# Performance work log

Hardware: AMD Instinct MI355X
Metric: run time of the kernel (lower is better)

## Reference

```python
import jax, jax.numpy as jnp
import numpy as np

B, L, T = 32, 256, 32
V_SIZE, D, H = 30000, 300, 256


def _gru(x, h0, Wih, Whh, bih, bhh):
    # x: [B,S,D], h0: [B,H]; PyTorch GRU gate order: r, z, n
    xg = jnp.einsum('bsd,gd->bsg', x, Wih) + bih  # [B,S,3H]

    def step(h, xg_t):
        gh = jnp.einsum('bh,gh->bg', h, Whh) + bhh
        ir, iz, in_ = jnp.split(xg_t, 3, axis=-1)
        hr, hz, hn_ = jnp.split(gh, 3, axis=-1)
        r = jax.nn.sigmoid(ir + hr)
        z = jax.nn.sigmoid(iz + hz)
        n = jnp.tanh(in_ + r * hn_)
        h_new = (1.0 - z) * n + z * h
        return h_new, h_new

    h_last, outs = jax.lax.scan(step, h0, jnp.swapaxes(xg, 0, 1))
    return jnp.swapaxes(outs, 0, 1), h_last  # [B,S,H], [B,H]


def setup_inputs() -> dict:
    rng = np.random.default_rng(0)
    Xin = rng.integers(0, V_SIZE, (B, L)).astype(np.int64)
    # strictly increasing segment ends; starts = previous end + 1
    Yindex = np.stack([np.sort(rng.choice(L, T, replace=False)) for _ in range(B)]).astype(np.int64)
    Xindex = np.concatenate([np.zeros((B, 1), np.int64), Yindex[:, :-1] + 1], axis=1)
    lens = np.full((B,), L, np.int64)
    s = 0.05
    p = lambda *shape: jnp.asarray(rng.standard_normal(shape) * s, jnp.float32)
    return {
        'Xin': jnp.asarray(Xin), 'Xindex': jnp.asarray(Xindex),
        'Yindex': jnp.asarray(Yindex), 'lens': jnp.asarray(lens),
        'emb': jnp.asarray(rng.standard_normal((V_SIZE, D)) * 0.1, jnp.float32),
        'Wih_e': p(3 * H, D), 'Whh_e': p(3 * H, H), 'bih_e': p(3 * H), 'bhh_e': p(3 * H),
        'Wih_d': p(3 * H, D), 'Whh_d': p(3 * H, H), 'bih_d': p(3 * H), 'bhh_d': p(3 * H),
        'W1': p(H, H), 'W2': p(H, H), 'Vv': p(H),
    }


def reference(Xin, Xindex, Yindex, lens, emb, Wih_e, Whh_e, bih_e, bhh_e,
              Wih_d, Whh_d, bih_d, bhh_d, W1, W2, Vv):
    # pointerEncoder (isbanor=False, dropout=0, lens==L so packed == plain)
    X = emb[Xin]                                   # [B,L,D]
    h0 = jnp.zeros((Xin.shape[0], Whh_e.shape[1]), X.dtype)
    hn, h_end = _gru(X, h0, Wih_e, Whh_e, bih_e, bhh_e)  # [B,L,H],[B,H]
    # training_decoder, vectorized over batch and decode steps
    dec_tok = jnp.take_along_axis(Xin, Xindex, axis=1)   # token ids at segment starts
    dx = emb[dec_tok]                              # [B,T,D]
    dout, _ = _gru(dx, h_end, Wih_d, Whh_d, bih_d, bhh_d)  # [B,T,H]
    # pointerLayer: v = selu(V . selu(W1 en + W2 d)), masked log_softmax over [start, curL)
    WE = jnp.einsum('blh,kh->blk', hn, W1)         # [B,L,H]
    WD = jnp.einsum('bth,kh->btk', dout, W2)       # [B,T,H]
    s = jax.nn.selu(WE[:, None, :, :] + WD[:, :, None, :])  # [B,T,L,H]
    v = jax.nn.selu(jnp.einsum('btlh,h->btl', s, Vv))        # [B,T,L]
    pos = jnp.arange(hn.shape[1])
    mask = (pos[None, None, :] >= Xindex[:, :, None]) & (pos[None, None, :] < lens[:, None, None])
    logits = jnp.where(mask, v, -jnp.inf)
    logp = jax.nn.log_softmax(logits, axis=-1)
    tgt_logp = jnp.take_along_axis(logp, Yindex[:, :, None], axis=-1)[..., 0]  # [B,T]
    return -jnp.mean(tgt_logp)  # batch_loss / LoopN
```

## Files before the change

kernel.cpp:

```cpp
#include <hip/hip_runtime.h>
#include <hip/hip_bf16.h>
#include <stdint.h>

#define B_  32
#define L_  256
#define T_  32
#define D_  300
#define H_  256
#define G3  768

__device__ __forceinline__ int sdot4(uint32_t a, uint32_t b, int acc) {
#if defined(__has_builtin) && __has_builtin(__builtin_amdgcn_sdot4)
  return __builtin_amdgcn_sdot4((int)a, (int)b, acc, false);
#else
  const int a0 = (int)(signed char)(a & 0xff),  b0 = (int)(signed char)(b & 0xff);
  const int a1 = (int)(signed char)((a >> 8) & 0xff),  b1 = (int)(signed char)((b >> 8) & 0xff);
  const int a2 = (int)(signed char)((a >> 16) & 0xff), b2 = (int)(signed char)((b >> 16) & 0xff);
  const int a3 = (int)(signed char)(a >> 24),          b3 = (int)(signed char)(b >> 24);
  return acc + a0 * b0 + a1 * b1 + a2 * b2 + a3 * b3;
#endif
}

__device__ __forceinline__ int sdot8(uint32_t a, uint32_t b, int acc) {
#if defined(__has_builtin) && __has_builtin(__builtin_amdgcn_sdot8)
  return __builtin_amdgcn_sdot8((int)a, (int)b, acc, false);
#else
  const uint32_t M = 0xF0F0F0F0u;
  const uint32_t alo = (a << 4) & M, ahi = a & M;
  const uint32_t blo = (b << 4) & M, bhi = b & M;
  return acc + ((sdot4(alo, blo, 0) + sdot4(ahi, bhi, 0)) >> 8);
#endif
}

__device__ __forceinline__ float rcp_f(float x) { return __builtin_amdgcn_rcpf(x); }
__device__ __forceinline__ float sigmoid_f(float x) { return rcp_f(1.0f + __expf(-x)); }
__device__ __forceinline__ float tanh_f(float x) {
  float e2 = __expf(2.0f * x);
  return 1.0f - 2.0f * rcp_f(e2 + 1.0f);
}
__device__ __forceinline__ uint16_t f2bf(float x) {
  uint32_t u = __builtin_bit_cast(uint32_t, x);
  return (uint16_t)((u + 0x7FFF + ((u >> 16) & 1)) >> 16);
}
__device__ __forceinline__ float bf2f(uint16_t b) {
  uint32_t u = ((uint32_t)b) << 16;
  return __builtin_bit_cast(float, u);
}

__device__ __forceinline__ void pack_body(int blk, const float* __restrict__ Whh,
                                          uint32_t* __restrict__ wQ,
                                          float* __restrict__ sw) {
  const int row = blk * 4 + (threadIdx.x >> 6);
  const int lane = threadIdx.x & 63;
  const float* wr = Whh + (long)row * H_;
  float m = 0.0f;
#pragma unroll
  for (int u = 0; u < 4; ++u) m = fmaxf(m, fabsf(wr[lane + 64 * u]));
  for (int off = 32; off > 0; off >>= 1) m = fmaxf(m, __shfl_xor(m, off, 64));
  const float inv = m > 0.0f ? 7.0f / m : 0.0f;
  if (lane == 0) sw[row] = m > 0.0f ? m / 49.0f : 0.0f;
  if (lane < 32) {
    const int pd = lane;
    uint32_t d = 0;
#pragma unroll
    for (int jn = 0; jn < 8; ++jn) {
      int v = __float2int_rn(wr[8 * pd + jn] * inv);
      v = v > 7 ? 7 : (v < -7 ? -7 : v);
      d |= ((uint32_t)(v & 0xF)) << (4 * jn);
    }
    wQ[(((size_t)(pd >> 2) * G3 + row) << 2) + (pd & 3)] = d;
  }
}

__device__ __forceinline__ void quant_body(int blk, const float* __restrict__ A,
                                           const int* __restrict__ rowidx,
                                           const int* __restrict__ Xin2,
                                           const int* __restrict__ Xidx2,
                                           uint32_t* __restrict__ out,
                                           float* __restrict__ scale,
                                           int M, int K, int Kd) {
  const int row = blk * 4 + (threadIdx.x >> 6);
  const int lane = threadIdx.x & 63;
  if (row >= M) return;
  long src = row;
  if (rowidx) src = rowidx[row];
  else if (Xin2) src = Xin2[(row >> 5) * L_ + Xidx2[row]];
  const float* ar = A + src * (long)K;
  float m = 0.0f;
  for (int e = lane; e < K; e += 64) m = fmaxf(m, fabsf(ar[e]));
  for (int off = 32; off > 0; off >>= 1) m = fmaxf(m, __shfl_xor(m, off, 64));
  const float inv = m > 0.0f ? 127.0f / m : 0.0f;
  if (lane == 0) scale[row] = m * (1.0f / 127.0f);
  for (int kd = lane; kd < Kd; kd += 64) {
    uint32_t d = 0;
#pragma unroll
    for (int u = 0; u < 4; ++u) {
      const int e = 4 * kd + u;
      int qv = (e < K) ? __float2int_rn(ar[e] * inv) : 0;
      qv = qv > 127 ? 127 : (qv < -127 ? -127 : qv);
      d |= ((uint32_t)(qv & 0xff)) << (8 * u);
    }
    out[(long)row * Kd + kd] = d;
  }
}

__device__ __forceinline__ void quant16(int blk, const float* __restrict__ A,
                                        uint32_t* __restrict__ out,
                                        float* __restrict__ scale,
                                        int M, int K, int Kd) {
  const int row = blk * 16 + (threadIdx.x >> 6);
  const int lane = threadIdx.x & 63;
  if (row >= M) return;
  const float* ar = A + (long)row * K;
  float m = 0.0f;
  for (int e = lane; e < K; e += 64) m = fmaxf(m, fabsf(ar[e]));
  for (int off = 32; off > 0; off >>= 1) m = fmaxf(m, __shfl_xor(m, off, 64));
  const float inv = m > 0.0f ? 127.0f / m : 0.0f;
  if (lane == 0) scale[row] = m * (1.0f / 127.0f);
  for (int kd = lane; kd < Kd; kd += 64) {
    uint32_t d = 0;
#pragma unroll
    for (int u = 0; u < 4; ++u) {
      const int e = 4 * kd + u;
      int qv = (e < K) ? __float2int_rn(ar[e] * inv) : 0;
      qv = qv > 127 ? 127 : (qv < -127 ? -127 : qv);
      d |= ((uint32_t)(qv & 0xff)) << (8 * u);
    }
    out[(long)row * Kd + kd] = d;
  }
}

__global__ __launch_bounds__(256)
void prep_all(const float* __restrict__ Whh_e, const float* __restrict__ Whh_d,
              uint32_t* __restrict__ wQ_e, uint32_t* __restrict__ wQ_d,
              float* __restrict__ sw_e, float* __restrict__ sw_d,
              const float* __restrict__ Wih_e, const float* __restrict__ Wih_d,
              uint32_t* __restrict__ WihQ_e, uint32_t* __restrict__ WihQ_d,
              float* __restrict__ sWih_e, float* __restrict__ sWih_d,
              const float* __restrict__ W1, const float* __restrict__ W2,
              uint32_t* __restrict__ W1q, uint32_t* __restrict__ W2q,
              float* __restrict__ sW1, float* __restrict__ sW2,
              const float* __restrict__ emb, const int* __restrict__ Xin,
              const int* __restrict__ Xindex,
              uint32_t* __restrict__ Aqe, float* __restrict__ saAe,
              uint32_t* __restrict__ Aqd, float* __restrict__ saAd,
              const float* __restrict__ bih_e, const float* __restrict__ bhh_e,
              float* __restrict__ bsum_e,
              const float* __restrict__ bih_d, const float* __restrict__ bhh_d,
              float* __restrict__ bsum_d) {
  const int blk = blockIdx.x;
  if (blk < 192)        pack_body(blk, Whh_e, wQ_e, sw_e);
  else if (blk < 384)   pack_body(blk - 192, Whh_d, wQ_d, sw_d);
  else if (blk < 576)   quant_body(blk - 384, Wih_e, nullptr, nullptr, nullptr,
                                   WihQ_e, sWih_e, 768, 300, 80);
  else if (blk < 768)   quant_body(blk - 576, Wih_d, nullptr, nullptr, nullptr,
                                   WihQ_d, sWih_d, 768, 300, 80);
  else if (blk < 832)   quant_body(blk - 768, W1, nullptr, nullptr, nullptr,
                                   W1q, sW1, 256, 256, 64);
  else if (blk < 896)   quant_body(blk - 832, W2, nullptr, nullptr, nullptr,
                                   W2q, sW2, 256, 256, 64);
  else if (blk < 2944)  quant_body(blk - 896, emb, Xin, nullptr, nullptr,
                                   Aqe, saAe, 8192, 300, 80);
  else if (blk < 3200)  quant_body(blk - 2944, emb, nullptr, Xin, Xindex,
                                   Aqd, saAd, 1024, 300, 80);
  else {
    const int blk2 = blk - 3200;
    const int i = (blk2 % 3) * 256 + threadIdx.x;
    const float* bih = blk2 < 3 ? bih_e : bih_d;
    const float* bhh = blk2 < 3 ? bhh_e : bhh_d;
    float* bsum = blk2 < 3 ? bsum_e : bsum_d;
    float v = bih[i];
    if (i < 2 * H_) v += bhh[i];
    bsum[i] = v;
  }
}

__device__ __forceinline__
void gemm_body(const uint32_t* __restrict__ Aq, const float* __restrict__ sa,
               const uint32_t* __restrict__ Wq, const float* __restrict__ swc,
               const float* __restrict__ bias, void* __restrict__ C,
               int bm, int bn, int M, int N, int Kd,
               bool transp, bool biasF, bool bf16out) {
  __shared__ uint32_t As[8][68];
  __shared__ uint32_t Ws[8][68];
  const int tid = threadIdx.x;
  const int ty = tid >> 4, tx = tid & 15;
  const int srow = tid >> 2;
  const int skd = (tid & 3) << 1;
  const uint32_t* Arow = Aq + (long)(bm * 64 + srow) * Kd + skd;
  const uint32_t* Wrow = Wq + (long)(bn * 64 + srow) * Kd + skd;
  int acc[4][4] = {};
  for (int k0 = 0; k0 < Kd; k0 += 8) {
    const uint32_t a0 = Arow[k0], a1 = Arow[k0 + 1];
    const uint32_t w0 = Wrow[k0], w1 = Wrow[k0 + 1];
    __syncthreads();
    As[skd][srow] = a0; As[skd + 1][srow] = a1;
    Ws[skd][srow] = w0; Ws[skd + 1][srow] = w1;
    __syncthreads();
#pragma unroll
    for (int kd = 0; kd < 8; ++kd) {
      const uint4 a4 = *(const uint4*)&As[kd][ty << 2];
      const uint4 b4 = *(const uint4*)&Ws[kd][tx << 2];
      acc[0][0] = sdot4(a4.x, b4.x, acc[0][0]);
      acc[0][1] = sdot4(a4.x, b4.y, acc[0][1]);
      acc[0][2] = sdot4(a4.x, b4.z, acc[0][2]);
      acc[0][3] = sdot4(a4.x, b4.w, acc[0][3]);
      acc[1][0] = sdot4(a4.y, b4.x, acc[1][0]);
      acc[1][1] = sdot4(a4.y, b4.y, acc[1][1]);
      acc[1][2] = sdot4(a4.y, b4.z, acc[1][2]);
      acc[1][3] = sdot4(a4.y, b4.w, acc[1][3]);
      acc[2][0] = sdot4(a4.z, b4.x, acc[2][0]);
      acc[2][1] = sdot4(a4.z, b4.y, acc[2][1]);
      acc[2][2] = sdot4(a4.z, b4.z, acc[2][2]);
      acc[2][3] = sdot4(a4.z, b4.w, acc[2][3]);
      acc[3][0] = sdot4(a4.w, b4.x, acc[3][0]);
      acc[3][1] = sdot4(a4.w, b4.y, acc[3][1]);
      acc[3][2] = sdot4(a4.w, b4.z, acc[3][2]);
      acc[3][3] = sdot4(a4.w, b4.w, acc[3][3]);
    }
  }
#pragma unroll
  for (int i = 0; i < 4; ++i) {
    const int m = bm * 64 + (ty << 2) + i;
    const float sai = sa[m];
#pragma unroll
    for (int j = 0; j < 4; ++j) {
      const int n = bn * 64 + (tx << 2) + j;
      float v = (float)acc[i][j] * sai * swc[n];
      if (biasF) v += bias[n];
      const long idx = transp ? ((((long)(m >> 8) * N + n) << 8) + (m & 255))
                              : ((long)m * N + n);
      if (bf16out) ((uint16_t*)C)[idx] = f2bf(v);
      else         ((float*)C)[idx] = v;
    }
  }
}

__global__ __launch_bounds__(256)
void xg_gemms(const uint32_t* __restrict__ Aqe, const float* __restrict__ saAe,
              const uint32_t* __restrict__ WihQ_e, const float* __restrict__ sWih_e,
              const float* __restrict__ bsum_e, uint16_t* __restrict__ xg_e,
              const uint32_t* __restrict__ Aqd, const float* __restrict__ saAd,
              const uint32_t* __restrict__ WihQ_d, const float* __restrict__ sWih_d,
              const float* __restrict__ bsum_d, uint16_t* __restrict__ xg_d) {
  const int blk = blockIdx.x;
  if (blk < 1536)
    gemm_body(Aqe, saAe, WihQ_e, sWih_e, bsum_e, xg_e,
              blk % 128, blk / 128, 8192, 768, 80, false, true, true);
  else {
    const int k = blk - 1536;
    gemm_body(Aqd, saAd, WihQ_d, sWih_d, bsum_d, xg_d,
              k % 16, k / 16, 1024, 768, 80, false, true, true);
  }
}


#define DOT8V(acc, p_, h_) { \
  acc = sdot8(p_.x, h_.x, acc); acc = sdot8(p_.y, h_.y, acc); \
  acc = sdot8(p_.z, h_.z, acc); acc = sdot8(p_.w, h_.w, acc); }

__device__ __forceinline__
void gru_block(int b, const uint16_t* __restrict__ xg, const uint4* __restrict__ wQv,
               const float* __restrict__ sw, const float* __restrict__ bhh,
               const float* __restrict__ h0, float* __restrict__ hout,
               float* __restrict__ hlast, int S,
               uint32_t (*h2)[32], int4 (*partv)[H_]) {
  const int tid = threadIdx.x;
  const int j = tid & 255;
  const int q = tid >> 8;
  const int base = (q * 2) * G3 + j;
  float bhn = 0.0f, h = 0.0f, swr = 0.0f, swz = 0.0f, swn = 0.0f;
  const uint16_t* xp = xg + (long)b * S * G3;
  float* hp_out = hout + (long)b * S * H_;
  if (q == 0) {
    bhn = bhh[2 * H_ + j];
    swr = sw[j]; swz = sw[H_ + j]; swn = sw[2 * H_ + j];
    h = h0 ? h0[b * H_ + j] : 0.0f;
    int hq4 = __float2int_rn(h * 7.0f);
    hq4 = hq4 > 7 ? 7 : (hq4 < -7 ? -7 : hq4);
    const int hq4n = __shfl_down(hq4, 1, 64);
    if (!(j & 1))
      ((uint8_t*)h2[0])[j >> 1] = (uint8_t)((hq4 & 0xF) | ((hq4n & 0xF) << 4));
  }
  __syncthreads();
  for (int t = 0; t < S; ++t) {
    const uint4* hq = (const uint4*)h2[t & 1] + q * 2;
    const uint4 ha = hq[0], hb = hq[1];
    float xr = 0.0f, xz = 0.0f, xn = 0.0f;
    if (q == 0) {
      xr = bf2f(xp[j]); xz = bf2f(xp[H_ + j]); xn = bf2f(xp[2 * H_ + j]);
    }
    int ar = 0, az = 0, an = 0;
    {
      const uint4 p0 = wQv[base], p1 = wQv[base + G3];
      DOT8V(ar, p0, ha) DOT8V(ar, p1, hb)
    }
    {
      const uint4 p0 = wQv[base + H_], p1 = wQv[base + G3 + H_];
      DOT8V(az, p0, ha) DOT8V(az, p1, hb)
    }
    {
      const uint4 p0 = wQv[base + 2 * H_], p1 = wQv[base + G3 + 2 * H_];
      DOT8V(an, p0, ha) DOT8V(an, p1, hb)
    }
    if (q) partv[q][j] = make_int4(ar, az, an, 0);
    __syncthreads();
    if (q == 0) {
      const int4 p1 = partv[1][j];
      const int4 p2 = partv[2][j];
      const int4 p3 = partv[3][j];
      const float arf = (float)(ar + p1.x + p2.x + p3.x) * swr;
      const float azf = (float)(az + p1.y + p2.y + p3.y) * swz;
      const float anf = (float)(an + p1.z + p2.z + p3.z) * swn;
      const float r = sigmoid_f(xr + arf);
      const float z = sigmoid_f(xz + azf);
      const float n = tanh_f(xn + r * (anf + bhn));
      h = (1.0f - z) * n + z * h;
      hp_out[j] = h;
      int hq4 = __float2int_rn(h * 7.0f);
      hq4 = hq4 > 7 ? 7 : (hq4 < -7 ? -7 : hq4);
      const int hq4n = __shfl_down(hq4, 1, 64);
      if (!(j & 1))
        ((uint8_t*)h2[(t & 1) ^ 1])[j >> 1] =
            (uint8_t)((hq4 & 0xF) | ((hq4n & 0xF) << 4));
    }
    xp += G3;
    hp_out += H_;
    __syncthreads();
  }
  if (q == 0 && hlast) hlast[b * H_ + j] = h;
}

__global__ __launch_bounds__(1024)
void gru_enc(const uint16_t* __restrict__ xg, const uint4* __restrict__ wQv,
             const float* __restrict__ sw, const float* __restrict__ bhh,
             float* __restrict__ hout, float* __restrict__ hlast, int S) {
  __shared__ __align__(16) uint32_t h2[2][32];
  __shared__ int4 partv[4][H_];
  gru_block(blockIdx.x, xg, wQv, sw, bhh, nullptr, hout, hlast, S, h2, partv);
}

__global__ __launch_bounds__(1024)
void dec_and_hquant(const uint16_t* __restrict__ xg_d, const uint4* __restrict__ wQ_d,
                    const float* __restrict__ sw_d, const float* __restrict__ bhh_d,
                    const float* __restrict__ hend, float* __restrict__ doutb,
                    const float* __restrict__ hn, uint32_t* __restrict__ hnq,
                    float* __restrict__ sahn) {
  __shared__ __align__(16) uint32_t h2[2][32];
  __shared__ int4 partv[4][H_];
  if (blockIdx.x < 32)
    gru_block(blockIdx.x, xg_d, wQ_d, sw_d, bhh_d, hend, doutb,
              (float*)nullptr, T_, h2, partv);
  else
    quant16(blockIdx.x - 32, hn, hnq, sahn, 8192, 256, 64);
}

__global__ __launch_bounds__(256)
void wet_and_dquant(const uint32_t* __restrict__ hnq, const float* __restrict__ sahn,
                    const uint32_t* __restrict__ W1q, const float* __restrict__ sW1,
                    float* __restrict__ WEt,
                    const float* __restrict__ doutb, uint32_t* __restrict__ dq,
                    float* __restrict__ sad) {
  if (blockIdx.x < 512)
    gemm_body(hnq, sahn, W1q, sW1, nullptr, WEt,
              blockIdx.x & 127, blockIdx.x >> 7, 8192, 256, 64, true, false, false);
  else
    quant_body(blockIdx.x - 512, doutb, nullptr, nullptr, nullptr,
               dq, sad, 1024, 256, 64);
}

__global__ __launch_bounds__(256)
void wd_gemm(const uint32_t* __restrict__ dq, const float* __restrict__ sad,
             const uint32_t* __restrict__ W2q, const float* __restrict__ sW2,
             float* __restrict__ WDb) {
  gemm_body(dq, sad, W2q, sW2, nullptr, WDb,
            blockIdx.x & 15, blockIdx.x >> 4, 1024, 256, 64, false, false, false);
}

__global__ __launch_bounds__(256)
void pointer_loss(const float* __restrict__ WEt, const float* __restrict__ WD,
                  const float* __restrict__ Vv,
                  const int* __restrict__ Xindex, const int* __restrict__ Yindex,
                  const int* __restrict__ lens, float* __restrict__ out) {
  const int t = blockIdx.x, b = blockIdx.y;
  const int l = threadIdx.x;
  __shared__ float wd_s[H_], vv_s[H_];
  __shared__ float rbuf[4], sbuf[4], vy_s;
  const int bt = b * T_ + t;
  wd_s[l] = WD[(long)bt * H_ + l];
  vv_s[l] = Vv[l] * 1.0507009873554805f;
  __syncthreads();
  const float* wet = WEt + (long)b * H_ * L_;
  const float alpha = 1.6732632423543772f;
  float acc = 0.0f;
#pragma unroll 4
  for (int hh = 0; hh < H_; ++hh) {
    const float xsum = wet[hh * L_ + l] + wd_s[hh];
    const float sneg = alpha * (__expf(xsum) - 1.0f);
    const float s = xsum > 0.0f ? xsum : sneg;
    acc = fmaf(s, vv_s[hh], acc);
  }
  float v;
  {
    const float sneg = alpha * (__expf(acc) - 1.0f);
    v = 1.0507009873554805f * (acc > 0.0f ? acc : sneg);
  }
  const int start = Xindex[bt];
  const int len = lens[b];
  const bool valid = (l >= start) && (l < len);
  const int y = Yindex[bt];
  if (l == y) vy_s = v;
  float m = valid ? v : -INFINITY;
  for (int off = 32; off > 0; off >>= 1) m = fmaxf(m, __shfl_xor(m, off, 64));
  const int wid = l >> 6, lane = l & 63;
  if (lane == 0) rbuf[wid] = m;
  __syncthreads();
  const float mx = fmaxf(fmaxf(rbuf[0], rbuf[1]), fmaxf(rbuf[2], rbuf[3]));
  float e = valid ? __expf(v - mx) : 0.0f;
  for (int off = 32; off > 0; off >>= 1) e += __shfl_xor(e, off, 64);
  if (lane == 0) sbuf[wid] = e;
  __syncthreads();
  if (l == 0) {
    const float sum = sbuf[0] + sbuf[1] + sbuf[2] + sbuf[3];
    atomicAdd(out, (mx + __logf(sum) - vy_s) * (1.0f / (B_ * T_)));
  }
}

extern "C" void kernel_launch(void* const* d_in, const int* in_sizes, int n_in,
                              void* d_out, int out_size, void* d_ws, size_t ws_size,
                              hipStream_t stream) {
  (void)in_sizes; (void)n_in; (void)out_size; (void)ws_size;
  const int*   Xin    = (const int*)d_in[0];
  const int*   Xindex = (const int*)d_in[1];
  const int*   Yindex = (const int*)d_in[2];
  const int*   lens   = (const int*)d_in[3];
  const float* emb    = (const float*)d_in[4];
  const float* Wih_e  = (const float*)d_in[5];
  const float* Whh_e  = (const float*)d_in[6];
  const float* bih_e  = (const float*)d_in[7];
  const float* bhh_e  = (const float*)d_in[8];
  const float* Wih_d  = (const float*)d_in[9];
  const float* Whh_d  = (const float*)d_in[10];
  const float* bih_d  = (const float*)d_in[11];
  const float* bhh_d  = (const float*)d_in[12];
  const float* W1     = (const float*)d_in[13];
  const float* W2     = (const float*)d_in[14];
  const float* Vv     = (const float*)d_in[15];

  char* p = (char*)d_ws;
  auto take = [&](size_t bytes) { void* q = (void*)p; p += (bytes + 255) & ~(size_t)255; return q; };
  uint32_t* wQ_e   = (uint32_t*)take((size_t)32 * G3 * 4);
  uint32_t* wQ_d   = (uint32_t*)take((size_t)32 * G3 * 4);
  float*    sw_e   = (float*)take((size_t)768 * 4);
  float*    sw_d   = (float*)take((size_t)768 * 4);
  uint32_t* WihQ_e = (uint32_t*)take((size_t)768 * 80 * 4);
  uint32_t* WihQ_d = (uint32_t*)take((size_t)768 * 80 * 4);
  float*    sWih_e = (float*)take((size_t)768 * 4);
  float*    sWih_d = (float*)take((size_t)768 * 4);
  uint32_t* W1q    = (uint32_t*)take((size_t)256 * 64 * 4);
  uint32_t* W2q    = (uint32_t*)take((size_t)256 * 64 * 4);
  float*    sW1    = (float*)take((size_t)256 * 4);
  float*    sW2    = (float*)take((size_t)256 * 4);
  float*    bsum_e = (float*)take((size_t)768 * 4);
  float*    bsum_d = (float*)take((size_t)768 * 4);
  uint16_t* xg_e   = (uint16_t*)take((size_t)8192 * 768 * 2);
  uint16_t* xg_d   = (uint16_t*)take((size_t)1024 * 768 * 2);
  float*    hn     = (float*)take((size_t)8192 * 256 * 4);
  float*    hend   = (float*)take((size_t)8192 * 4);
  float*    doutb  = (float*)take((size_t)1024 * 256 * 4);
  float*    WDb    = (float*)take((size_t)1024 * 256 * 4);
  float*    WEt    = (float*)take((size_t)8192 * 256 * 4);
  uint32_t* Aqe    = (uint32_t*)take((size_t)8192 * 80 * 4);
  float*    saAe   = (float*)take((size_t)8192 * 4);
  uint32_t* Aqd    = (uint32_t*)take((size_t)1024 * 80 * 4);
  float*    saAd   = (float*)take((size_t)1024 * 4);
  uint32_t* hnq  = Aqe;
  float*    sahn = saAe;
  uint32_t* dq   = Aqd;
  float*    sad  = saAd;

  hipMemsetAsync(d_out, 0, sizeof(float), stream);

  hipLaunchKernelGGL(prep_all, dim3(3206), dim3(256), 0, stream,
                     Whh_e, Whh_d, wQ_e, wQ_d, sw_e, sw_d,
                     Wih_e, Wih_d, WihQ_e, WihQ_d, sWih_e, sWih_d,
                     W1, W2, W1q, W2q, sW1, sW2,
                     emb, Xin, Xindex, Aqe, saAe, Aqd, saAd,
                     bih_e, bhh_e, bsum_e, bih_d, bhh_d, bsum_d);

  hipLaunchKernelGGL(xg_gemms, dim3(1728), dim3(256), 0, stream,
                     Aqe, saAe, WihQ_e, sWih_e, bsum_e, xg_e,
                     Aqd, saAd, WihQ_d, sWih_d, bsum_d, xg_d);

  hipLaunchKernelGGL(gru_enc, dim3(32), dim3(1024), 0, stream,
                     xg_e, (const uint4*)wQ_e, sw_e, bhh_e, hn, hend, L_);

  hipLaunchKernelGGL(dec_and_hquant, dim3(544), dim3(1024), 0, stream,
                     xg_d, (const uint4*)wQ_d, sw_d, bhh_d, hend, doutb,
                     hn, hnq, sahn);

  hipLaunchKernelGGL(wet_and_dquant, dim3(768), dim3(256), 0, stream,
                     hnq, sahn, W1q, sW1, WEt, doutb, dq, sad);

  hipLaunchKernelGGL(wd_gemm, dim3(64), dim3(256), 0, stream,
                     dq, sad, W2q, sW2, WDb);

  hipLaunchKernelGGL(pointer_loss, dim3(T_, B_), dim3(256), 0, stream,
                     WEt, WDb, Vv, Xindex, Yindex, lens, (float*)d_out);
}
```

Before: 285.8 us.

## Double-buffer GRU weight registers and use LDS-only barriers in recurrent loop

Unrolls the GRU time loop by two and ping-pongs two register sets of quantized Whh weights, issuing the next step's weight loads before the current step's dot products. This hides global or L2 load latency behind compute. Barriers now wait only on lgkmcnt before s_barrier, so outstanding global loads need not drain at each sync. A large unused shared array in the encoder kernel limits occupancy to one block per CU, likely to give each sequential GRU block its own CU. The weights are loop-invariant, so the repeated loads are redundant but kept, and the unroll assumes S is even.

```diff
diff --git a/kernel.cpp b/kernel.cpp
--- a/kernel.cpp
+++ b/kernel.cpp
@@ -259,6 +259,49 @@
   acc = sdot8(p_.x, h_.x, acc); acc = sdot8(p_.y, h_.y, acc); \
   acc = sdot8(p_.z, h_.z, acc); acc = sdot8(p_.w, h_.w, acc); }
 
+#define LGKM_BARRIER() { \
+  asm volatile("s_waitcnt lgkmcnt(0)" ::: "memory"); \
+  __builtin_amdgcn_s_barrier(); }
+
+#define GRU_STEP(CUR, NXT, TT) { \
+  NXT##r0 = wp[0];        NXT##r1 = wp[G3]; \
+  NXT##z0 = wp[H_];       NXT##z1 = wp[G3 + H_]; \
+  NXT##n0 = wp[2 * H_];   NXT##n1 = wp[G3 + 2 * H_]; \
+  const uint4* hq_ = (const uint4*)h2[(TT) & 1] + q * 2; \
+  const uint4 ha_ = hq_[0], hb_ = hq_[1]; \
+  float xr_ = 0.0f, xz_ = 0.0f, xn_ = 0.0f; \
+  if (q == 0) { \
+    xr_ = bf2f(xp[j]); xz_ = bf2f(xp[H_ + j]); xn_ = bf2f(xp[2 * H_ + j]); \
+  } \
+  int ar_ = 0, az_ = 0, an_ = 0; \
+  DOT8V(ar_, CUR##r0, ha_) DOT8V(ar_, CUR##r1, hb_) \
+  DOT8V(az_, CUR##z0, ha_) DOT8V(az_, CUR##z1, hb_) \
+  DOT8V(an_, CUR##n0, ha_) DOT8V(an_, CUR##n1, hb_) \
+  if (q) partv[q][j] = make_int4(ar_, az_, an_, 0); \
+  LGKM_BARRIER(); \
+  if (q == 0) { \
+    const int4 p1_ = partv[1][j]; \
+    const int4 p2_ = partv[2][j]; \
+    const int4 p3_ = partv[3][j]; \
+    const float arf_ = (float)(ar_ + p1_.x + p2_.x + p3_.x) * swr; \
+    const float azf_ = (float)(az_ + p1_.y + p2_.y + p3_.y) * swz; \
+    const float anf_ = (float)(an_ + p1_.z + p2_.z + p3_.z) * swn; \
+    const float r_ = sigmoid_f(xr_ + arf_); \
+    const float z_ = sigmoid_f(xz_ + azf_); \
+    const float n_ = tanh_f(xn_ + r_ * (anf_ + bhn)); \
+    h = (1.0f - z_) * n_ + z_ * h; \
+    hp_out[j] = h; \
+    int hq4_ = __float2int_rn(h * 7.0f); \
+    hq4_ = hq4_ > 7 ? 7 : (hq4_ < -7 ? -7 : hq4_); \
+    const int hq4n_ = __shfl_down(hq4_, 1, 64); \
+    if (!(j & 1)) \
+      ((uint8_t*)h2[((TT) & 1) ^ 1])[j >> 1] = \
+          (uint8_t)((hq4_ & 0xF) | ((hq4n_ & 0xF) << 4)); \
+  } \
+  xp += G3; \
+  hp_out += H_; \
+  LGKM_BARRIER(); }
+
 __device__ __forceinline__
 void gru_block(int b, const uint16_t* __restrict__ xg, const uint4* __restrict__ wQv,
                const float* __restrict__ sw, const float* __restrict__ bhh,
@@ -268,7 +311,7 @@
   const int tid = threadIdx.x;
   const int j = tid & 255;
   const int q = tid >> 8;
-  const int base = (q * 2) * G3 + j;
+  const uint4* wp = wQv + (q * 2) * G3 + j;
   float bhn = 0.0f, h = 0.0f, swr = 0.0f, swz = 0.0f, swn = 0.0f;
   const uint16_t* xp = xg + (long)b * S * G3;
   float* hp_out = hout + (long)b * S * H_;
@@ -282,51 +325,14 @@
     if (!(j & 1))
       ((uint8_t*)h2[0])[j >> 1] = (uint8_t)((hq4 & 0xF) | ((hq4n & 0xF) << 4));
   }
+  uint4 uAr0 = wp[0],      uAr1 = wp[G3];
+  uint4 uAz0 = wp[H_],     uAz1 = wp[G3 + H_];
+  uint4 uAn0 = wp[2 * H_], uAn1 = wp[G3 + 2 * H_];
+  uint4 uBr0, uBr1, uBz0, uBz1, uBn0, uBn1;
   __syncthreads();
-  for (int t = 0; t < S; ++t) {
-    const uint4* hq = (const uint4*)h2[t & 1] + q * 2;
-    const uint4 ha = hq[0], hb = hq[1];
-    float xr = 0.0f, xz = 0.0f, xn = 0.0f;
-    if (q == 0) {
-      xr = bf2f(xp[j]); xz = bf2f(xp[H_ + j]); xn = bf2f(xp[2 * H_ + j]);
-    }
-    int ar = 0, az = 0, an = 0;
-    {
-      const uint4 p0 = wQv[base], p1 = wQv[base + G3];
-      DOT8V(ar, p0, ha) DOT8V(ar, p1, hb)
-    }
-    {
-      const uint4 p0 = wQv[base + H_], p1 = wQv[base + G3 + H_];
-      DOT8V(az, p0, ha) DOT8V(az, p1, hb)
-    }
-    {
-      const uint4 p0 = wQv[base + 2 * H_], p1 = wQv[base + G3 + 2 * H_];
-      DOT8V(an, p0, ha) DOT8V(an, p1, hb)
-    }
-    if (q) partv[q][j] = make_int4(ar, az, an, 0);
-    __syncthreads();
-    if (q == 0) {
-      const int4 p1 = partv[1][j];
-      const int4 p2 = partv[2][j];
-      const int4 p3 = partv[3][j];
-      const float arf = (float)(ar + p1.x + p2.x + p3.x) * swr;
-      const float azf = (float)(az + p1.y + p2.y + p3.y) * swz;
-      const float anf = (float)(an + p1.z + p2.z + p3.z) * swn;
-      const float r = sigmoid_f(xr + arf);
-      const float z = sigmoid_f(xz + azf);
-      const float n = tanh_f(xn + r * (anf + bhn));
-      h = (1.0f - z) * n + z * h;
-      hp_out[j] = h;
-      int hq4 = __float2int_rn(h * 7.0f);
-      hq4 = hq4 > 7 ? 7 : (hq4 < -7 ? -7 : hq4);
-      const int hq4n = __shfl_down(hq4, 1, 64);
-      if (!(j & 1))
-        ((uint8_t*)h2[(t & 1) ^ 1])[j >> 1] =
-            (uint8_t)((hq4 & 0xF) | ((hq4n & 0xF) << 4));
-    }
-    xp += G3;
-    hp_out += H_;
-    __syncthreads();
+  for (int t = 0; t < S; t += 2) {
+    GRU_STEP(uA, uB, t)
+    GRU_STEP(uB, uA, t + 1)
   }
   if (q == 0 && hlast) hlast[b * H_ + j] = h;
 }
@@ -337,6 +343,8 @@
              float* __restrict__ hout, float* __restrict__ hlast, int S) {
   __shared__ __align__(16) uint32_t h2[2][32];
   __shared__ int4 partv[4][H_];
+  __shared__ uint4 occ_pad[4160];
+  if (S < 0) occ_pad[0] = make_uint4(0, 0, 0, 0);
   gru_block(blockIdx.x, xg, wQv, sw, bhh, nullptr, hout, hlast, S, h2, partv);
 }
 
```

Result: no change. 288.2 us (+0.9%).
